# Kernel tuning notes

Measured on AMD Instinct MI355X. Metric: run time of the kernel, lower is better.

## Reference

```python
import jax, jax.numpy as jnp
import numpy as np

EPS = 1e-06

def feature_map(x):
    # elu(x) + 1
    return jax.nn.elu(x) + 1.0

def setup_inputs() -> dict:
    key = jax.random.key(0)
    kq, kk, kv = jax.random.split(key, 3)
    N, L, S, H, D = 8, 8192, 8192, 8, 32
    queries = jax.random.normal(kq, (N, L, H, D), dtype=jnp.float32)
    keys = jax.random.normal(kk, (N, S, H, D), dtype=jnp.float32)
    values = jax.random.normal(kv, (N, S, H, D), dtype=jnp.float32)
    return {"queries": queries, "keys": keys, "values": values}

def reference(queries, keys, values):
    # Linear attention ("Transformers are RNNs"), faithful to forward_linear.
    Q = feature_map(queries)          # [N, L, H, D]
    K = feature_map(keys)             # [N, S, H, D]
    v_length = values.shape[1]
    vals = values / v_length          # [N, S, H, Dv]
    KV = jnp.einsum('nshd,nshv->nhdv', K, vals)            # [N, H, D, Dv]
    Z = 1.0 / (jnp.einsum('nlhd,nhd->nlh', Q, K.sum(axis=1)) + EPS)  # [N, L, H]
    out = jnp.einsum('nlhd,nhdv,nlh->nlhv', Q, KV, Z) * v_length     # [N, L, H, Dv]
    return out
```

## Files before the change

### kernel.cpp

```cpp
#include <hip/hip_runtime.h>


#define L_Q 8192
#define S_K 8192
#define DIM 32
#define RS 256
#define EPSV 1e-6f
#define NPAIR 64
#define WSFLOATS (NPAIR * 1056)

__device__ __forceinline__ float fmap(float x) {
    return x > 0.0f ? x + 1.0f : __expf(x);
}

#define CHUNKS 32
#define SROWS (S_K / CHUNKS)
#define A_ITERS (SROWS / 32)
#define SKP 36

union SmemA {
    struct { float K[4][8][SKP]; float V[4][8][SKP]; } st;
    struct { float red[4][64][16]; float redk[4][32]; } rd;
};

__global__ __launch_bounds__(256, 5) void kv_kernel(const float* __restrict__ Kg,
                                                    const float* __restrict__ Vg,
                                                    float* __restrict__ ws)
{
    __shared__ SmemA sm;
    const int pair = blockIdx.y;
    const int n = pair >> 3, h = pair & 7;
    const int t = threadIdx.x;
    const int w = t >> 6;
    const int l = t & 63;
    const int g = l >> 4;
    const int i = l & 15;
    const int db = i >> 2;
    const int vb = i & 3;

    const int srow = l >> 3;
    const int scol = (l & 7) * 4;

    const size_t base = ((size_t)n * S_K + (size_t)blockIdx.x * SROWS) * RS
                      + (size_t)h * DIM;
    size_t gaddr = base + (size_t)(w * 8 + srow) * RS + scol;

    float acc[8][8];
    float ksum[8];
    #pragma unroll
    for (int a = 0; a < 8; ++a) {
        ksum[a] = 0.0f;
        #pragma unroll
        for (int b = 0; b < 8; ++b) acc[a][b] = 0.0f;
    }

    float4 pK = *(const float4*)(Kg + gaddr);
    float4 pV = *(const float4*)(Vg + gaddr);

    float (*sK)[SKP] = sm.st.K[w];
    float (*sV)[SKP] = sm.st.V[w];

    for (int it = 0; it < A_ITERS; ++it) {
        float4 a = pK;
        a.x = fmap(a.x); a.y = fmap(a.y); a.z = fmap(a.z); a.w = fmap(a.w);
        *(float4*)(&sK[srow][scol]) = a;
        *(float4*)(&sV[srow][scol]) = pV;
        if (it + 1 < A_ITERS) {
            gaddr += (size_t)32 * RS;
            pK = *(const float4*)(Kg + gaddr);
            pV = *(const float4*)(Vg + gaddr);
        }
        #pragma unroll
        for (int rr = 0; rr < 2; ++rr) {
            const int r = 2 * g + rr;
            const float4 k0 = *(const float4*)&sK[r][db * 8];
            const float4 k1 = *(const float4*)&sK[r][db * 8 + 4];
            const float4 v0 = *(const float4*)&sV[r][vb * 8];
            const float4 v1 = *(const float4*)&sV[r][vb * 8 + 4];
            const float kk[8] = {k0.x,k0.y,k0.z,k0.w,k1.x,k1.y,k1.z,k1.w};
            const float vv[8] = {v0.x,v0.y,v0.z,v0.w,v1.x,v1.y,v1.z,v1.w};
            #pragma unroll
            for (int a2 = 0; a2 < 8; ++a2) {
                ksum[a2] += kk[a2];
                #pragma unroll
                for (int b2 = 0; b2 < 8; ++b2) acc[a2][b2] += kk[a2] * vv[b2];
            }
        }
    }

    #pragma unroll
    for (int a = 0; a < 8; ++a) {
        #pragma unroll
        for (int b = 0; b < 8; ++b) {
            acc[a][b] += __shfl_xor(acc[a][b], 16);
            acc[a][b] += __shfl_xor(acc[a][b], 32);
        }
        ksum[a] += __shfl_xor(ksum[a], 16);
        ksum[a] += __shfl_xor(ksum[a], 32);
    }
    __syncthreads();
    if (l < 16) {
        #pragma unroll
        for (int a = 0; a < 8; ++a)
            #pragma unroll
            for (int b = 0; b < 8; ++b)
                sm.rd.red[w][a * 8 + b][i] = acc[a][b];
        if (vb == 0) {
            #pragma unroll
            for (int a = 0; a < 8; ++a) sm.rd.redk[w][db * 8 + a] = ksum[a];
        }
    }
    __syncthreads();
    float* KVp = ws + pair * 1056;
    #pragma unroll
    for (int p = t; p < 1024; p += 256) {
        const int kIdx = p >> 4, iIdx = p & 15;
        const float v = sm.rd.red[0][kIdx][iIdx] + sm.rd.red[1][kIdx][iIdx]
                      + sm.rd.red[2][kIdx][iIdx] + sm.rd.red[3][kIdx][iIdx];
        const int d  = ((iIdx >> 2) << 3) + (kIdx >> 3);
        const int vv = ((iIdx & 3) << 3) + (kIdx & 7);
        unsafeAtomicAdd(&KVp[d * DIM + vv], v);
    }
    if (t < 32) {
        const float v = sm.rd.redk[0][t] + sm.rd.redk[1][t]
                      + sm.rd.redk[2][t] + sm.rd.redk[3][t];
        unsafeAtomicAdd(&KVp[1024 + t], v);
    }
}

#define BROWS 128
#define TP 132

__global__ __launch_bounds__(256, 8) void out_kernel(const float* __restrict__ Q,
                                                     const float* __restrict__ ws,
                                                     float* __restrict__ out)
{
    __shared__ float sQt[DIM][TP];
    __shared__ float sKV[DIM][DIM];
    __shared__ float sKs[DIM];

    const int pair = blockIdx.y;
    const int n = pair >> 3, h = pair & 7;
    const int t = threadIdx.x;
    const int w = t >> 6, l = t & 63;
    const int vb = l & 7;
    const int rb = l >> 3;

    const float* wp = ws + pair * 1056;
    for (int p = t; p < 1024; p += 256) (&sKV[0][0])[p] = wp[p];
    if (t < DIM) sKs[t] = wp[1024 + t];

    const size_t qbase = ((size_t)n * L_Q + (size_t)blockIdx.x * BROWS) * RS
                       + (size_t)h * DIM;

    {
        const int r = t >> 1;
        const int half = (t & 1) * 16;
        const float* qp = Q + qbase + (size_t)r * RS + half;
        #pragma unroll
        for (int j = 0; j < 4; ++j) {
            const float4 v = *(const float4*)(qp + j * 4);
            sQt[half + j * 4 + 0][r] = fmap(v.x);
            sQt[half + j * 4 + 1][r] = fmap(v.y);
            sQt[half + j * 4 + 2][r] = fmap(v.z);
            sQt[half + j * 4 + 3][r] = fmap(v.w);
        }
    }
    __syncthreads();

    const int rowbase = w * 32 + rb * 4;
    float acc[4][4];
    float den[4] = {0.0f, 0.0f, 0.0f, 0.0f};
    #pragma unroll
    for (int j = 0; j < 4; ++j)
        #pragma unroll
        for (int b = 0; b < 4; ++b) acc[j][b] = 0.0f;

    #pragma unroll
    for (int d = 0; d < DIM; ++d) {
        const float4 q4 = *(const float4*)&sQt[d][rowbase];
        const float ksd = sKs[d];
        const float4 c = *(const float4*)&sKV[d][vb * 4];
        const float qq[4] = {q4.x, q4.y, q4.z, q4.w};
        const float cc[4] = {c.x, c.y, c.z, c.w};
        #pragma unroll
        for (int j = 0; j < 4; ++j) {
            den[j] += qq[j] * ksd;
            #pragma unroll
            for (int b = 0; b < 4; ++b) acc[j][b] += qq[j] * cc[b];
        }
    }

    #pragma unroll
    for (int j = 0; j < 4; ++j) {
        const float z = 1.0f / (den[j] + EPSV);
        float4 o;
        o.x = acc[j][0] * z; o.y = acc[j][1] * z;
        o.z = acc[j][2] * z; o.w = acc[j][3] * z;
        *(float4*)(out + qbase + (size_t)(rowbase + j) * RS + vb * 4) = o;
    }
}

extern "C" void kernel_launch(void* const* d_in, const int* in_sizes, int n_in,
                              void* d_out, int out_size, void* d_ws, size_t ws_size,
                              hipStream_t stream)
{
    const float* Q = (const float*)d_in[0];
    const float* K = (const float*)d_in[1];
    const float* V = (const float*)d_in[2];
    float* outp = (float*)d_out;
    float* ws = (float*)d_ws;

    hipMemsetAsync(d_ws, 0, WSFLOATS * sizeof(float), stream);

    dim3 gA(CHUNKS, NPAIR);
    kv_kernel<<<gA, 256, 0, stream>>>(K, V, ws);

    dim3 gB(L_Q / BROWS, NPAIR);
    out_kernel<<<gB, 256, 0, stream>>>(Q, ws, outp);
}
```

Baseline: 274.4 us.

## Process all heads per block with full-row loads and deterministic partial reduction

Both kernels now have each block cover all 8 heads of a batch item, loading contiguous full 256-float rows as float4 instead of 32-float per-head slices. The atomic accumulation and memset are replaced by per-chunk partial KV buffers plus a separate reduce kernel. The output kernel loops over four 32-row tiles with register prefetch of Q. This targets poorly coalesced strided head accesses and atomic traffic, at the cost of an extra kernel launch and workspace round trip.

After: 239.0 us. 12.9% less time.

```diff
diff --git a/kernel.cpp b/kernel.cpp
--- a/kernel.cpp
+++ b/kernel.cpp
@@ -1,203 +1,215 @@
 #include <hip/hip_runtime.h>
 
 
-#define L_Q 8192
-#define S_K 8192
-#define DIM 32
-#define RS 256
+#define RS4 64
 #define EPSV 1e-6f
-#define NPAIR 64
-#define WSFLOATS (NPAIR * 1056)
+
+#define KV_CH 32
+#define KV_ROWS 256
+#define KV_TILE 16
+#define KV_ITERS 16
+#define PH4 264
+#define FIN4 (8 * KV_CH * 8 * PH4)
+
+#define KP 67
+#define OP 67
+#define KVP 265
 
 __device__ __forceinline__ float fmap(float x) {
     return x > 0.0f ? x + 1.0f : __expf(x);
 }
-
-#define CHUNKS 32
-#define SROWS (S_K / CHUNKS)
-#define A_ITERS (SROWS / 32)
-#define SKP 36
-
-union SmemA {
-    struct { float K[4][8][SKP]; float V[4][8][SKP]; } st;
-    struct { float red[4][64][16]; float redk[4][32]; } rd;
-};
-
-__global__ __launch_bounds__(256, 5) void kv_kernel(const float* __restrict__ Kg,
-                                                    const float* __restrict__ Vg,
-                                                    float* __restrict__ ws)
-{
-    __shared__ SmemA sm;
-    const int pair = blockIdx.y;
+__device__ __forceinline__ float4 fmap4(float4 v) {
+    return make_float4(fmap(v.x), fmap(v.y), fmap(v.z), fmap(v.w));
+}
+__device__ __forceinline__ float f4c(const float4& v, int i) {
+    return i == 0 ? v.x : i == 1 ? v.y : i == 2 ? v.z : v.w;
+}
+
+__global__ __launch_bounds__(256) void kv_kernel(const float4* __restrict__ Kg,
+                                                 const float4* __restrict__ Vg,
+                                                 float4* __restrict__ ws)
+{
+    __shared__ float4 sK[2][KV_TILE * KP];
+    __shared__ float4 sV[2][KV_TILE * KP];
+
+    const int n = blockIdx.y, c = blockIdx.x;
+    const int t = threadIdx.x;
+    const int h = t >> 5;
+    const int q = t & 31;
+    const int dq = (q >> 3) * 2;
+    const int vs = q & 7;
+
+    size_t gbase = ((size_t)n * 8192 + (size_t)c * KV_ROWS) * RS4 + t;
+
+    float acc[8][4];
+    float ksum[8];
+    #pragma unroll
+    for (int a = 0; a < 8; ++a) {
+        ksum[a] = 0.0f;
+        acc[a][0] = acc[a][1] = acc[a][2] = acc[a][3] = 0.0f;
+    }
+
+    float4 pK[4], pV[4];
+    #pragma unroll
+    for (int k = 0; k < 4; ++k) { pK[k] = Kg[gbase + k * 256]; pV[k] = Vg[gbase + k * 256]; }
+
+    for (int it = 0; it < KV_ITERS; ++it) {
+        float4* bK = sK[it & 1];
+        float4* bV = sV[it & 1];
+        #pragma unroll
+        for (int k = 0; k < 4; ++k) {
+            const int idx = k * 256 + t;
+            const int dst = (idx >> 6) * KP + (idx & 63);
+            bK[dst] = fmap4(pK[k]);
+            bV[dst] = pV[k];
+        }
+        if (it + 1 < KV_ITERS) {
+            gbase += (size_t)KV_TILE * RS4;
+            #pragma unroll
+            for (int k = 0; k < 4; ++k) { pK[k] = Kg[gbase + k * 256]; pV[k] = Vg[gbase + k * 256]; }
+        }
+        __syncthreads();
+        #pragma unroll
+        for (int r = 0; r < KV_TILE; ++r) {
+            const float4 k0 = bK[r * KP + h * 8 + dq];
+            const float4 k1 = bK[r * KP + h * 8 + dq + 1];
+            const float4 v  = bV[r * KP + h * 8 + vs];
+            const float kk[8] = {k0.x, k0.y, k0.z, k0.w, k1.x, k1.y, k1.z, k1.w};
+            #pragma unroll
+            for (int a = 0; a < 8; ++a) {
+                ksum[a]   += kk[a];
+                acc[a][0] += kk[a] * v.x;
+                acc[a][1] += kk[a] * v.y;
+                acc[a][2] += kk[a] * v.z;
+                acc[a][3] += kk[a] * v.w;
+            }
+        }
+    }
+
+    const size_t pb = ((size_t)(n * KV_CH + c) * 8 + h) * PH4;
+    const int d0 = (q >> 3) * 8;
+    #pragma unroll
+    for (int a = 0; a < 8; ++a)
+        ws[pb + (size_t)(d0 + a) * 8 + vs] =
+            make_float4(acc[a][0], acc[a][1], acc[a][2], acc[a][3]);
+    if (vs == 0) {
+        ws[pb + 256 + dq]     = make_float4(ksum[0], ksum[1], ksum[2], ksum[3]);
+        ws[pb + 256 + dq + 1] = make_float4(ksum[4], ksum[5], ksum[6], ksum[7]);
+    }
+}
+
+__global__ __launch_bounds__(256) void reduce_kernel(float4* __restrict__ ws)
+{
+    const int pair = blockIdx.x;
     const int n = pair >> 3, h = pair & 7;
     const int t = threadIdx.x;
-    const int w = t >> 6;
-    const int l = t & 63;
-    const int g = l >> 4;
-    const int i = l & 15;
-    const int db = i >> 2;
-    const int vb = i & 3;
-
-    const int srow = l >> 3;
-    const int scol = (l & 7) * 4;
-
-    const size_t base = ((size_t)n * S_K + (size_t)blockIdx.x * SROWS) * RS
-                      + (size_t)h * DIM;
-    size_t gaddr = base + (size_t)(w * 8 + srow) * RS + scol;
-
-    float acc[8][8];
-    float ksum[8];
-    #pragma unroll
-    for (int a = 0; a < 8; ++a) {
-        ksum[a] = 0.0f;
-        #pragma unroll
-        for (int b = 0; b < 8; ++b) acc[a][b] = 0.0f;
-    }
-
-    float4 pK = *(const float4*)(Kg + gaddr);
-    float4 pV = *(const float4*)(Vg + gaddr);
-
-    float (*sK)[SKP] = sm.st.K[w];
-    float (*sV)[SKP] = sm.st.V[w];
-
-    for (int it = 0; it < A_ITERS; ++it) {
-        float4 a = pK;
-        a.x = fmap(a.x); a.y = fmap(a.y); a.z = fmap(a.z); a.w = fmap(a.w);
-        *(float4*)(&sK[srow][scol]) = a;
-        *(float4*)(&sV[srow][scol]) = pV;
-        if (it + 1 < A_ITERS) {
-            gaddr += (size_t)32 * RS;
-            pK = *(const float4*)(Kg + gaddr);
-            pV = *(const float4*)(Vg + gaddr);
-        }
-        #pragma unroll
-        for (int rr = 0; rr < 2; ++rr) {
-            const int r = 2 * g + rr;
-            const float4 k0 = *(const float4*)&sK[r][db * 8];
-            const float4 k1 = *(const float4*)&sK[r][db * 8 + 4];
-            const float4 v0 = *(const float4*)&sV[r][vb * 8];
-            const float4 v1 = *(const float4*)&sV[r][vb * 8 + 4];
-            const float kk[8] = {k0.x,k0.y,k0.z,k0.w,k1.x,k1.y,k1.z,k1.w};
-            const float vv[8] = {v0.x,v0.y,v0.z,v0.w,v1.x,v1.y,v1.z,v1.w};
-            #pragma unroll
-            for (int a2 = 0; a2 < 8; ++a2) {
-                ksum[a2] += kk[a2];
+    const size_t cs = 8 * PH4;
+
+    for (int e = t; e < PH4; e += 256) {
+        const size_t b = ((size_t)(n * KV_CH) * 8 + h) * PH4 + e;
+        float4 s0 = make_float4(0.f, 0.f, 0.f, 0.f), s1 = s0, s2 = s0, s3 = s0;
+        #pragma unroll
+        for (int c = 0; c < KV_CH; c += 4) {
+            const float4 a0 = ws[b + (size_t)(c + 0) * cs];
+            const float4 a1 = ws[b + (size_t)(c + 1) * cs];
+            const float4 a2 = ws[b + (size_t)(c + 2) * cs];
+            const float4 a3 = ws[b + (size_t)(c + 3) * cs];
+            s0.x += a0.x; s0.y += a0.y; s0.z += a0.z; s0.w += a0.w;
+            s1.x += a1.x; s1.y += a1.y; s1.z += a1.z; s1.w += a1.w;
+            s2.x += a2.x; s2.y += a2.y; s2.z += a2.z; s2.w += a2.w;
+            s3.x += a3.x; s3.y += a3.y; s3.z += a3.z; s3.w += a3.w;
+        }
+        ws[FIN4 + (size_t)pair * PH4 + e] =
+            make_float4(s0.x + s1.x + s2.x + s3.x, s0.y + s1.y + s2.y + s3.y,
+                        s0.z + s1.z + s2.z + s3.z, s0.w + s1.w + s2.w + s3.w);
+    }
+}
+
+__global__ __launch_bounds__(256) void out_kernel(const float4* __restrict__ Q,
+                                                  const float4* __restrict__ ws,
+                                                  float4* __restrict__ out)
+{
+    __shared__ float4 sKV[8 * KVP];
+    __shared__ float4 sQ[32 * OP];
+
+    const int n = blockIdx.y, cL = blockIdx.x;
+    const int t = threadIdx.x;
+    const int h = t >> 5;
+    const int q = t & 31;
+    const int rblk = q >> 3;
+    const int vs = q & 7;
+
+    size_t gbase = ((size_t)n * 8192 + (size_t)cL * 128) * RS4 + t;
+
+    float4 pf[8];
+    #pragma unroll
+    for (int k = 0; k < 8; ++k) pf[k] = Q[gbase + k * 256];
+
+    {
+        const size_t fb = FIN4 + (size_t)n * 8 * PH4;
+        #pragma unroll
+        for (int k = 0; k < 9; ++k) {
+            const int p = k * 256 + t;
+            if (p < 8 * PH4) {
+                const int hh = p / PH4, e = p - hh * PH4;
+                sKV[hh * KVP + e] = ws[fb + p];
+            }
+        }
+    }
+
+    for (int it = 0; it < 4; ++it) {
+        __syncthreads();
+        #pragma unroll
+        for (int k = 0; k < 8; ++k) {
+            const int idx = k * 256 + t;
+            sQ[(idx >> 6) * OP + (idx & 63)] = fmap4(pf[k]);
+        }
+        if (it + 1 < 4) {
+            gbase += (size_t)32 * RS4;
+            #pragma unroll
+            for (int k = 0; k < 8; ++k) pf[k] = Q[gbase + k * 256];
+        }
+        __syncthreads();
+
+        float acc[8][4];
+        float den[8];
+        #pragma unroll
+        for (int j = 0; j < 8; ++j) {
+            den[j] = 0.0f;
+            acc[j][0] = acc[j][1] = acc[j][2] = acc[j][3] = 0.0f;
+        }
+
+        #pragma unroll
+        for (int dc = 0; dc < 8; ++dc) {
+            const float4 ks = sKV[h * KVP + 256 + dc];
+            float4 qr[8];
+            #pragma unroll
+            for (int j = 0; j < 8; ++j)
+                qr[j] = sQ[(rblk + 4 * j) * OP + h * 8 + dc];
+            #pragma unroll
+            for (int dd = 0; dd < 4; ++dd) {
+                const float4 kv = sKV[h * KVP + (dc * 4 + dd) * 8 + vs];
+                const float ksd = f4c(ks, dd);
                 #pragma unroll
-                for (int b2 = 0; b2 < 8; ++b2) acc[a2][b2] += kk[a2] * vv[b2];
+                for (int j = 0; j < 8; ++j) {
+                    const float qv = f4c(qr[j], dd);
+                    acc[j][0] += qv * kv.x;
+                    acc[j][1] += qv * kv.y;
+                    acc[j][2] += qv * kv.z;
+                    acc[j][3] += qv * kv.w;
+                    den[j]    += qv * ksd;
+                }
             }
         }
-    }
-
-    #pragma unroll
-    for (int a = 0; a < 8; ++a) {
-        #pragma unroll
-        for (int b = 0; b < 8; ++b) {
-            acc[a][b] += __shfl_xor(acc[a][b], 16);
-            acc[a][b] += __shfl_xor(acc[a][b], 32);
-        }
-        ksum[a] += __shfl_xor(ksum[a], 16);
-        ksum[a] += __shfl_xor(ksum[a], 32);
-    }
-    __syncthreads();
-    if (l < 16) {
-        #pragma unroll
-        for (int a = 0; a < 8; ++a)
-            #pragma unroll
-            for (int b = 0; b < 8; ++b)
-                sm.rd.red[w][a * 8 + b][i] = acc[a][b];
-        if (vb == 0) {
-            #pragma unroll
-            for (int a = 0; a < 8; ++a) sm.rd.redk[w][db * 8 + a] = ksum[a];
-        }
-    }
-    __syncthreads();
-    float* KVp = ws + pair * 1056;
-    #pragma unroll
-    for (int p = t; p < 1024; p += 256) {
-        const int kIdx = p >> 4, iIdx = p & 15;
-        const float v = sm.rd.red[0][kIdx][iIdx] + sm.rd.red[1][kIdx][iIdx]
-                      + sm.rd.red[2][kIdx][iIdx] + sm.rd.red[3][kIdx][iIdx];
-        const int d  = ((iIdx >> 2) << 3) + (kIdx >> 3);
-        const int vv = ((iIdx & 3) << 3) + (kIdx & 7);
-        unsafeAtomicAdd(&KVp[d * DIM + vv], v);
-    }
-    if (t < 32) {
-        const float v = sm.rd.redk[0][t] + sm.rd.redk[1][t]
-                      + sm.rd.redk[2][t] + sm.rd.redk[3][t];
-        unsafeAtomicAdd(&KVp[1024 + t], v);
-    }
-}
-
-#define BROWS 128
-#define TP 132
-
-__global__ __launch_bounds__(256, 8) void out_kernel(const float* __restrict__ Q,
-                                                     const float* __restrict__ ws,
-                                                     float* __restrict__ out)
-{
-    __shared__ float sQt[DIM][TP];
-    __shared__ float sKV[DIM][DIM];
-    __shared__ float sKs[DIM];
-
-    const int pair = blockIdx.y;
-    const int n = pair >> 3, h = pair & 7;
-    const int t = threadIdx.x;
-    const int w = t >> 6, l = t & 63;
-    const int vb = l & 7;
-    const int rb = l >> 3;
-
-    const float* wp = ws + pair * 1056;
-    for (int p = t; p < 1024; p += 256) (&sKV[0][0])[p] = wp[p];
-    if (t < DIM) sKs[t] = wp[1024 + t];
-
-    const size_t qbase = ((size_t)n * L_Q + (size_t)blockIdx.x * BROWS) * RS
-                       + (size_t)h * DIM;
-
-    {
-        const int r = t >> 1;
-        const int half = (t & 1) * 16;
-        const float* qp = Q + qbase + (size_t)r * RS + half;
-        #pragma unroll
-        for (int j = 0; j < 4; ++j) {
-            const float4 v = *(const float4*)(qp + j * 4);
-            sQt[half + j * 4 + 0][r] = fmap(v.x);
-            sQt[half + j * 4 + 1][r] = fmap(v.y);
-            sQt[half + j * 4 + 2][r] = fmap(v.z);
-            sQt[half + j * 4 + 3][r] = fmap(v.w);
-        }
-    }
-    __syncthreads();
-
-    const int rowbase = w * 32 + rb * 4;
-    float acc[4][4];
-    float den[4] = {0.0f, 0.0f, 0.0f, 0.0f};
-    #pragma unroll
-    for (int j = 0; j < 4; ++j)
-        #pragma unroll
-        for (int b = 0; b < 4; ++b) acc[j][b] = 0.0f;
-
-    #pragma unroll
-    for (int d = 0; d < DIM; ++d) {
-        const float4 q4 = *(const float4*)&sQt[d][rowbase];
-        const float ksd = sKs[d];
-        const float4 c = *(const float4*)&sKV[d][vb * 4];
-        const float qq[4] = {q4.x, q4.y, q4.z, q4.w};
-        const float cc[4] = {c.x, c.y, c.z, c.w};
-        #pragma unroll
-        for (int j = 0; j < 4; ++j) {
-            den[j] += qq[j] * ksd;
-            #pragma unroll
-            for (int b = 0; b < 4; ++b) acc[j][b] += qq[j] * cc[b];
-        }
-    }
-
-    #pragma unroll
-    for (int j = 0; j < 4; ++j) {
-        const float z = 1.0f / (den[j] + EPSV);
-        float4 o;
-        o.x = acc[j][0] * z; o.y = acc[j][1] * z;
-        o.z = acc[j][2] * z; o.w = acc[j][3] * z;
-        *(float4*)(out + qbase + (size_t)(rowbase + j) * RS + vb * 4) = o;
+
+        const size_t ob = ((size_t)n * 8192 + (size_t)cL * 128 + it * 32 + rblk) * RS4
+                        + h * 8 + vs;
+        #pragma unroll
+        for (int j = 0; j < 8; ++j) {
+            const float z = 1.0f / (den[j] + EPSV);
+            out[ob + (size_t)(4 * j) * RS4] =
+                make_float4(acc[j][0] * z, acc[j][1] * z, acc[j][2] * z, acc[j][3] * z);
+        }
     }
 }
 
@@ -205,17 +217,18 @@
                               void* d_out, int out_size, void* d_ws, size_t ws_size,
                               hipStream_t stream)
 {
-    const float* Q = (const float*)d_in[0];
-    const float* K = (const float*)d_in[1];
-    const float* V = (const float*)d_in[2];
-    float* outp = (float*)d_out;
-    float* ws = (float*)d_ws;
-
-    hipMemsetAsync(d_ws, 0, WSFLOATS * sizeof(float), stream);
-
-    dim3 gA(CHUNKS, NPAIR);
+    const float4* Q = (const float4*)d_in[0];
+    const float4* K = (const float4*)d_in[1];
+    const float4* V = (const float4*)d_in[2];
+    float4* outp = (float4*)d_out;
+    float4* ws = (float4*)d_ws;
+
+
+    dim3 gA(KV_CH, 8);
     kv_kernel<<<gA, 256, 0, stream>>>(K, V, ws);
 
-    dim3 gB(L_Q / BROWS, NPAIR);
+    reduce_kernel<<<64, 256, 0, stream>>>(ws);
+
+    dim3 gB(64, 8);
     out_kernel<<<gB, 256, 0, stream>>>(Q, ws, outp);
 }
```
